# Optimization experiments

Hardware: AMD Instinct MI355X
Metric: run time of the kernel (lower is better)

Reference implementation:

```python
import jax, jax.numpy as jnp
import numpy as np

N_HEAD = 12
N_EMBD = 768

def setup_inputs() -> dict:
    key = jax.random.key(0)
    ks = jax.random.split(key, 5)
    B, T, C = 4, 2048, N_EMBD
    x = jax.random.normal(ks[0], (B, T, C), dtype=jnp.float32)
    # c_attn: Linear(C, 3C); c_proj: Linear(C, C). Torch Linear stores W as [out,in].
    w_attn = jax.random.normal(ks[1], (3 * C, C), dtype=jnp.float32) * (1.0 / np.sqrt(C))
    b_attn = jnp.zeros((3 * C,), dtype=jnp.float32)
    w_proj = jax.random.normal(ks[2], (C, C), dtype=jnp.float32) * (1.0 / np.sqrt(C))
    b_proj = jnp.zeros((C,), dtype=jnp.float32)
    return {"x": x, "w_attn": w_attn, "b_attn": b_attn, "w_proj": w_proj, "b_proj": b_proj}

def reference(x, w_attn, b_attn, w_proj, b_proj):
    B, T, C = x.shape
    H = N_HEAD
    hs = C // H
    qkv = jnp.einsum('btc,oc->bto', x, w_attn) + b_attn  # [B,T,3C]
    q, k, v = jnp.split(qkv, 3, axis=-1)
    # [B,T,C] -> [B,H,T,hs]
    q = q.reshape(B, T, H, hs).transpose(0, 2, 1, 3)
    k = k.reshape(B, T, H, hs).transpose(0, 2, 1, 3)
    v = v.reshape(B, T, H, hs).transpose(0, 2, 1, 3)
    scale = 1.0 / np.sqrt(hs)
    att = jnp.einsum('bhqd,bhkd->bhqk', q, k) * scale  # [B,H,T,T]
    causal = jnp.tril(jnp.ones((T, T), dtype=bool))
    att = jnp.where(causal[None, None], att, -jnp.inf)
    att = jax.nn.softmax(att, axis=-1)
    y = jnp.einsum('bhqk,bhkd->bhqd', att, v)  # [B,H,T,hs]
    y = y.transpose(0, 2, 1, 3).reshape(B, T, C)
    return jnp.einsum('btc,oc->bto', y, w_proj) + b_proj
```

## Files before the change

### kernel.cpp

```cpp
#include <hip/hip_runtime.h>
#include <hip/hip_bf16.h>


typedef __attribute__((ext_vector_type(8))) short bf16x8;
typedef __attribute__((ext_vector_type(4))) short bf16x4;
typedef __attribute__((ext_vector_type(4))) float f32x4;

#define MFMA16(a, b, c) __builtin_amdgcn_mfma_f32_16x16x32_bf16((a), (b), (c), 0, 0, 0)

__device__ __forceinline__ unsigned short f2bfbits(float f) {
  return __builtin_bit_cast(unsigned short, __float2bfloat16(f));
}
__device__ __forceinline__ float bf2f(short b) {
  return __uint_as_float(((unsigned)(unsigned short)b) << 16);
}
__device__ __forceinline__ float fast_exp2(float x) {
#if __has_builtin(__builtin_amdgcn_exp2f)
  return __builtin_amdgcn_exp2f(x);
#else
  return __expf(x * 0.6931471805599453f);
#endif
}
__device__ __forceinline__ float fmax3(float a, float b, float c) {
  return fmaxf(fmaxf(a, b), c);
}
__device__ __forceinline__ unsigned pk2bf(float lo, float hi) {
  return (__builtin_bit_cast(unsigned, hi) & 0xffff0000u) |
         (__builtin_bit_cast(unsigned, lo) >> 16);
}

__device__ __forceinline__ void gload_lds16(const void* g, void* l) {
  __builtin_amdgcn_global_load_lds((const __attribute__((address_space(1))) void*)g,
                                   (__attribute__((address_space(3))) void*)l, 16, 0, 0);
}

__global__ __launch_bounds__(256) void cvt3(const float* __restrict__ x,
                                            const float* __restrict__ wa,
                                            const float* __restrict__ wp,
                                            unsigned short* __restrict__ xb,
                                            unsigned short* __restrict__ wab,
                                            unsigned short* __restrict__ wpb) {
  int i = blockIdx.x * 256 + threadIdx.x;
  const float* in;
  unsigned short* out;
  int j;
  if (i < 1572864) { in = x; out = xb; j = i; }
  else if (i < 2015232) { in = wa; out = wab; j = i - 1572864; }
  else { in = wp; out = wpb; j = i - 2015232; }
  float4 f = ((const float4*)in)[j];
  bf16x4 o;
  o[0] = (short)f2bfbits(f.x); o[1] = (short)f2bfbits(f.y);
  o[2] = (short)f2bfbits(f.z); o[3] = (short)f2bfbits(f.w);
  ((bf16x4*)out)[j] = o;
}

template <typename OutT>
__global__ __launch_bounds__(256) void gemm_bt(const unsigned short* __restrict__ A,
                                               const unsigned short* __restrict__ Bt,
                                               const float* __restrict__ bias,
                                               OutT* __restrict__ C, int M, int N, int K,
                                               int nx, int cpx) {
  __shared__ unsigned short As[128 * 64];
  __shared__ unsigned short Bs[128 * 64];
  const int tid = threadIdx.x;
  const int w = tid >> 6, l = tid & 63;
  const int g = l >> 4, li = l & 15;
  const int wm = w >> 1, wn = w & 1;

  const int bid = blockIdx.x;
  const int swz = (bid & 7) * cpx + (bid >> 3);
  const int bx = swz % nx, by = swz / nx;
  const int m0 = by * 128, n0 = bx * 128;

  const int scw = (l & 7) ^ ((l >> 3) & 7);
  const int swr = li & 7;

  f32x4 acc[4][4] = {};

  for (int kt = 0; kt < K; kt += 64) {
#pragma unroll
    for (int n = 0; n < 4; ++n) {
      int R = w * 32 + n * 8 + (l >> 3);
      gload_lds16(A + (long)(m0 + R) * K + kt + scw * 8, &As[(w * 32 + n * 8) * 64]);
      gload_lds16(Bt + (long)(n0 + R) * K + kt + scw * 8, &Bs[(w * 32 + n * 8) * 64]);
    }
    __syncthreads();
#pragma unroll
    for (int kk = 0; kk < 2; ++kk) {
      bf16x8 a[4], b[4];
#pragma unroll
      for (int m = 0; m < 4; ++m)
        a[m] = *(const bf16x8*)&As[(wm * 64 + m * 16 + li) * 64 + ((kk * 4 + g) ^ swr) * 8];
#pragma unroll
      for (int n = 0; n < 4; ++n)
        b[n] = *(const bf16x8*)&Bs[(wn * 64 + n * 16 + li) * 64 + ((kk * 4 + g) ^ swr) * 8];
#pragma unroll
      for (int m = 0; m < 4; ++m)
#pragma unroll
        for (int n = 0; n < 4; ++n) acc[m][n] = MFMA16(a[m], b[n], acc[m][n]);
    }
    __syncthreads();
  }

#pragma unroll
  for (int m = 0; m < 4; ++m) {
    int row = m0 + wm * 64 + m * 16 + 4 * g;
#pragma unroll
    for (int n = 0; n < 4; ++n) {
      int col = n0 + wn * 64 + n * 16 + li;
      float bi = bias[col];
#pragma unroll
      for (int r = 0; r < 4; ++r) {
        float v = acc[m][n][r] + bi;
        if constexpr (sizeof(OutT) == 2)
          C[(long)(row + r) * N + col] = (OutT)f2bfbits(v);
        else
          C[(long)(row + r) * N + col] = v;
      }
    }
  }
}

__global__ __launch_bounds__(64) void transpose_v(const unsigned short* __restrict__ qkv,
                                                  unsigned short* __restrict__ vt) {
  const int kt = blockIdx.x & 31, bh = blockIdx.x >> 5;
  const int b = bh / 12, h = bh - b * 12;
  const int l = threadIdx.x;
  const int ct = l & 7, cd = l >> 3;

  bf16x8 tin[8], tout[8];
#pragma unroll
  for (int i = 0; i < 8; ++i)
    tin[i] = *(const bf16x8*)(qkv + (long)(b * 2048 + kt * 64 + ct * 8 + i) * 2304 +
                              1536 + h * 64 + cd * 8);
#pragma unroll
  for (int j = 0; j < 8; ++j) {
#pragma unroll
    for (int i = 0; i < 8; ++i) tout[j][i] = tin[i][j];
    *(bf16x8*)(vt + (long)(bh * 64 + cd * 8 + j) * 2048 + kt * 64 + ct * 8) = tout[j];
  }
}

__device__ __forceinline__ bf16x8 scale_bf8(bf16x8 v, float c) {
  bf16x8 o;
#pragma unroll
  for (int j = 0; j < 8; ++j) o[j] = (short)f2bfbits(bf2f(v[j]) * c);
  return o;
}

__device__ __forceinline__ void softmax_state(f32x4* s, bool diag, int g, int li, int qloc,
                                              unsigned short* PsW, float& m, f32x4* o,
                                              f32x4& o4) {
  if (diag) {
#pragma unroll
    for (int kn = 0; kn < 4; ++kn)
#pragma unroll
      for (int r = 0; r < 4; ++r)
        if (kn * 16 + 4 * g + r > qloc) s[kn][r] = -1e30f;
  }
  float a = fmax3(s[0][0], s[0][1], s[0][2]);
  float b = fmax3(s[0][3], s[1][0], s[1][1]);
  float c = fmax3(s[1][2], s[1][3], s[2][0]);
  float d = fmax3(s[2][1], s[2][2], s[2][3]);
  float e = fmax3(s[3][0], s[3][1], s[3][2]);
  float pm = fmaxf(fmax3(a, b, c), fmax3(d, e, s[3][3]));
  pm = fmaxf(pm, __shfl_xor(pm, 16));
  pm = fmaxf(pm, __shfl_xor(pm, 32));

  if (!__all(pm - m <= 10.0f)) {
    float mn = fmaxf(m, pm);
    float alpha = fast_exp2(m - mn);
    m = mn;
    float alo[4];
#pragma unroll
    for (int r = 0; r < 4; ++r) alo[r] = __shfl(alpha, 20 * g + r);
#pragma unroll
    for (int dn = 0; dn < 4; ++dn)
#pragma unroll
      for (int r = 0; r < 4; ++r) o[dn][r] *= alo[r];
#pragma unroll
    for (int r = 0; r < 4; ++r) o4[r] *= alo[r];
  }

  const int swp = li & 7;
#pragma unroll
  for (int kn = 0; kn < 4; ++kn) {
    float e0 = fast_exp2(s[kn][0] - m);
    float e1 = fast_exp2(s[kn][1] - m);
    float e2 = fast_exp2(s[kn][2] - m);
    float e3 = fast_exp2(s[kn][3] - m);
    uint2 pk = {pk2bf(e0, e1), pk2bf(e2, e3)};
    *(uint2*)&PsW[li * 64 + ((kn * 2 + (g >> 1)) ^ swp) * 8 + (g & 1) * 4] = pk;
  }
}

template <bool DUAL>
__device__ __forceinline__ void attn_tile(const unsigned short* Ks, const unsigned short* Vs,
                                          unsigned short* PsH, unsigned short* PsL,
                                          const bf16x8* bqh, const bf16x8* bql,
                                          bool diagh, bool diagl, int g, int li, int qloc,
                                          float& mh, f32x4* oh, f32x4& oh4,
                                          float& ml, f32x4* ol, f32x4& ol4) {
  f32x4 sh[4], sl[4];
  __builtin_amdgcn_s_setprio(1);
#pragma unroll
  for (int kn = 0; kn < 4; ++kn) {
    int rr = kn * 16 + li, sw = rr & 7;
    f32x4 ah = {}, al = {};
#pragma unroll
    for (int kk = 0; kk < 2; ++kk) {
      bf16x8 ak = *(const bf16x8*)&Ks[rr * 64 + ((kk * 4 + g) ^ sw) * 8];
      ah = MFMA16(ak, bqh[kk], ah);
      if constexpr (DUAL) al = MFMA16(ak, bql[kk], al);
    }
    sh[kn] = ah;
    if constexpr (DUAL) sl[kn] = al;
  }
  __builtin_amdgcn_s_setprio(0);

  softmax_state(sh, diagh, g, li, qloc, PsH, mh, oh, oh4);
  if constexpr (DUAL) softmax_state(sl, diagl, g, li, qloc, PsL, ml, ol, ol4);

  bf16x8 vones;
#pragma unroll
  for (int j = 0; j < 8; ++j) vones[j] = (short)0x3F80;

  const int swp = li & 7;
  __builtin_amdgcn_s_setprio(1);
#pragma unroll
  for (int kk = 0; kk < 2; ++kk) {
    bf16x8 pah = *(const bf16x8*)&PsH[li * 64 + ((kk * 4 + g) ^ swp) * 8];
    bf16x8 pal;
    if constexpr (DUAL) pal = *(const bf16x8*)&PsL[li * 64 + ((kk * 4 + g) ^ swp) * 8];
#pragma unroll
    for (int dn = 0; dn < 4; ++dn) {
      int rv = dn * 16 + li;
      bf16x8 vb = *(const bf16x8*)&Vs[rv * 64 + ((kk * 4 + g) ^ (rv & 7)) * 8];
      oh[dn] = MFMA16(pah, vb, oh[dn]);
      if constexpr (DUAL) ol[dn] = MFMA16(pal, vb, ol[dn]);
    }
    oh4 = MFMA16(pah, vones, oh4);
    if constexpr (DUAL) ol4 = MFMA16(pal, vones, ol4);
  }
  __builtin_amdgcn_s_setprio(0);
}

__global__ __launch_bounds__(256, 3) void attn_fwd(const unsigned short* __restrict__ qkv,
                                                   const unsigned short* __restrict__ vt,
                                                   unsigned short* __restrict__ y) {
  const int orig = (blockIdx.x & 7) * 96 + (blockIdx.x >> 3);
  const int bh = orig >> 4, p = orig & 15;
  const int b = bh / 12, h = bh - b * 12;
  const int qlo = p, qhi = 31 - p;
  const int tid = threadIdx.x;
  const int w = tid >> 6, l = tid & 63;
  const int g = l >> 4, li = l & 15;
  const int qloc = w * 16 + li;

  __shared__ unsigned short Ks[2][64 * 64];
  __shared__ unsigned short Vs[2][64 * 64];
  __shared__ unsigned short Ps[8][16 * 64];
  unsigned short* PsH = &Ps[w][0];
  unsigned short* PsL = &Ps[4 + w][0];

  const unsigned short* base = qkv + (long)b * 2048 * 2304;

  const float QS = 0.18033688011112042f;
  bf16x8 bqlo[2], bqhi[2];
  {
    const unsigned short* qr = base + (long)(qlo * 64 + qloc) * 2304 + h * 64;
    bqlo[0] = scale_bf8(*(const bf16x8*)(qr + 8 * g), QS);
    bqlo[1] = scale_bf8(*(const bf16x8*)(qr + 32 + 8 * g), QS);
    qr = base + (long)(qhi * 64 + qloc) * 2304 + h * 64;
    bqhi[0] = scale_bf8(*(const bf16x8*)(qr + 8 * g), QS);
    bqhi[1] = scale_bf8(*(const bf16x8*)(qr + 32 + 8 * g), QS);
  }

  float m_lo = -1e30f, m_hi = -1e30f;
  f32x4 o_lo[4] = {}, o_hi[4] = {};
  f32x4 o4_lo = {}, o4_hi = {};

  const int sR = w * 8 + (l >> 3);
  const int sc = l & 7;

  int buf = 0;
  {
#pragma unroll
    for (int n = 0; n < 2; ++n) {
      int R = n * 32 + sR;
      int c = sc ^ (R & 7);
      gload_lds16(base + (long)R * 2304 + 768 + h * 64 + c * 8, &Ks[0][(n * 32 + w * 8) * 64]);
      gload_lds16(vt + (long)(bh * 64 + R) * 2048 + c * 8, &Vs[0][(n * 32 + w * 8) * 64]);
    }
  }
  __syncthreads();

  for (int kt = 0; kt <= qhi; ++kt) {
    if (kt < qhi) {
#pragma unroll
      for (int n = 0; n < 2; ++n) {
        int R = n * 32 + sR;
        int c = sc ^ (R & 7);
        gload_lds16(base + (long)((kt + 1) * 64 + R) * 2304 + 768 + h * 64 + c * 8,
                    &Ks[buf ^ 1][(n * 32 + w * 8) * 64]);
        gload_lds16(vt + (long)(bh * 64 + R) * 2048 + (kt + 1) * 64 + c * 8,
                    &Vs[buf ^ 1][(n * 32 + w * 8) * 64]);
      }
    }
    if (kt <= qlo)
      attn_tile<true>(Ks[buf], Vs[buf], PsH, PsL, bqhi, bqlo, kt == qhi, kt == qlo,
                      g, li, qloc, m_hi, o_hi, o4_hi, m_lo, o_lo, o4_lo);
    else
      attn_tile<false>(Ks[buf], Vs[buf], PsH, PsL, bqhi, bqlo, kt == qhi, false,
                       g, li, qloc, m_hi, o_hi, o4_hi, m_lo, o_lo, o4_lo);
    __syncthreads();
    buf ^= 1;
  }

#pragma unroll
  for (int t = 0; t < 2; ++t) {
    const f32x4* o = t ? o_hi : o_lo;
    const f32x4& o4 = t ? o4_hi : o4_lo;
    int qt = t ? qhi : qlo;
#pragma unroll
    for (int r = 0; r < 4; ++r) {
      float inv = 1.0f / o4[r];
      long row = (long)b * 2048 + qt * 64 + w * 16 + 4 * g + r;
#pragma unroll
      for (int dn = 0; dn < 4; ++dn)
        y[row * 768 + h * 64 + dn * 16 + li] = (unsigned short)f2bfbits(o[dn][r] * inv);
    }
  }
}

extern "C" void kernel_launch(void* const* d_in, const int* in_sizes, int n_in,
                              void* d_out, int out_size, void* d_ws, size_t ws_size,
                              hipStream_t stream) {
  const float* x      = (const float*)d_in[0];
  const float* w_attn = (const float*)d_in[1];
  const float* b_attn = (const float*)d_in[2];
  const float* w_proj = (const float*)d_in[3];
  const float* b_proj = (const float*)d_in[4];
  float* out = (float*)d_out;

  unsigned short* xb   = (unsigned short*)d_ws;
  unsigned short* wab  = xb + 6291456;
  unsigned short* wpb  = wab + 1769472;
  unsigned short* qkvb = wpb + 589824;
  unsigned short* yb   = qkvb + (long)8192 * 2304;
  unsigned short* vtb  = yb + 6291456;

  cvt3<<<8448, 256, 0, stream>>>(x, w_attn, w_proj, xb, wab, wpb);

  gemm_bt<unsigned short><<<1152, 256, 0, stream>>>(xb, wab, b_attn, qkvb, 8192, 2304, 768, 18, 144);
  transpose_v<<<1536, 64, 0, stream>>>(qkvb, vtb);
  attn_fwd<<<768, 256, 0, stream>>>(qkvb, vtb, yb);
  gemm_bt<float><<<384, 256, 0, stream>>>(yb, wpb, b_proj, out, 8192, 768, 768, 6, 48);
}
```

Before: 135.4 us.

## Fuse V transpose into QKV GEMM epilogue and remap attention block schedule

The QKV GEMM epilogue now writes V-column tiles straight into the transposed V layout, so the separate transpose kernel and its extra read/write of V are gone. The attention kernel's block-to-(head, query-pair) mapping is also changed: each XCD now gets six contiguous heads, and the query-pair index is rotated to spread the causal workload. The fused epilogue writes 4-element bf16 chunks along the time axis, which may coalesce less well than the old writes.

```diff
diff --git a/kernel.cpp b/kernel.cpp
--- a/kernel.cpp
+++ b/kernel.cpp
@@ -54,12 +54,13 @@
   ((bf16x4*)out)[j] = o;
 }
 
-template <typename OutT>
+template <typename OutT, bool VFUSE>
 __global__ __launch_bounds__(256) void gemm_bt(const unsigned short* __restrict__ A,
                                                const unsigned short* __restrict__ Bt,
                                                const float* __restrict__ bias,
-                                               OutT* __restrict__ C, int M, int N, int K,
-                                               int nx, int cpx) {
+                                               OutT* __restrict__ C,
+                                               unsigned short* __restrict__ vt,
+                                               int M, int N, int K, int nx, int cpx) {
   __shared__ unsigned short As[128 * 64];
   __shared__ unsigned short Bs[128 * 64];
   const int tid = threadIdx.x;
@@ -100,6 +101,29 @@
         for (int n = 0; n < 4; ++n) acc[m][n] = MFMA16(a[m], b[n], acc[m][n]);
     }
     __syncthreads();
+  }
+
+  if constexpr (VFUSE) {
+    if (n0 >= 1536) {
+      const int b = m0 >> 11;
+      const int t0b = (m0 & 2047) + wm * 64;
+#pragma unroll
+      for (int n = 0; n < 4; ++n) {
+        int col = n0 + wn * 64 + n * 16 + li;
+        int h = (col - 1536) >> 6, d = (col - 1536) & 63;
+        float bi = bias[col];
+        long vrow = ((long)(b * 12 + h) * 64 + d) * 2048;
+#pragma unroll
+        for (int m = 0; m < 4; ++m) {
+          int t0 = t0b + m * 16 + 4 * g;
+          bf16x4 pk;
+#pragma unroll
+          for (int r = 0; r < 4; ++r) pk[r] = (short)f2bfbits(acc[m][n][r] + bi);
+          *(bf16x4*)&vt[vrow + t0] = pk;
+        }
+      }
+      return;
+    }
   }
 
 #pragma unroll
@@ -118,26 +142,6 @@
           C[(long)(row + r) * N + col] = v;
       }
     }
-  }
-}
-
-__global__ __launch_bounds__(64) void transpose_v(const unsigned short* __restrict__ qkv,
-                                                  unsigned short* __restrict__ vt) {
-  const int kt = blockIdx.x & 31, bh = blockIdx.x >> 5;
-  const int b = bh / 12, h = bh - b * 12;
-  const int l = threadIdx.x;
-  const int ct = l & 7, cd = l >> 3;
-
-  bf16x8 tin[8], tout[8];
-#pragma unroll
-  for (int i = 0; i < 8; ++i)
-    tin[i] = *(const bf16x8*)(qkv + (long)(b * 2048 + kt * 64 + ct * 8 + i) * 2304 +
-                              1536 + h * 64 + cd * 8);
-#pragma unroll
-  for (int j = 0; j < 8; ++j) {
-#pragma unroll
-    for (int i = 0; i < 8; ++i) tout[j][i] = tin[i][j];
-    *(bf16x8*)(vt + (long)(bh * 64 + cd * 8 + j) * 2048 + kt * 64 + ct * 8) = tout[j];
   }
 }
 
@@ -248,8 +252,10 @@
 __global__ __launch_bounds__(256, 3) void attn_fwd(const unsigned short* __restrict__ qkv,
                                                    const unsigned short* __restrict__ vt,
                                                    unsigned short* __restrict__ y) {
-  const int orig = (blockIdx.x & 7) * 96 + (blockIdx.x >> 3);
-  const int bh = orig >> 4, p = orig & 15;
+  const int xcd = blockIdx.x & 7;
+  const int slot = blockIdx.x >> 3;
+  const int bh = xcd * 6 + (slot >> 4);
+  const int p = ((slot & 15) + 11 * (slot >> 5)) & 15;
   const int b = bh / 12, h = bh - b * 12;
   const int qlo = p, qhi = 31 - p;
   const int tid = threadIdx.x;
@@ -352,8 +358,9 @@
 
   cvt3<<<8448, 256, 0, stream>>>(x, w_attn, w_proj, xb, wab, wpb);
 
-  gemm_bt<unsigned short><<<1152, 256, 0, stream>>>(xb, wab, b_attn, qkvb, 8192, 2304, 768, 18, 144);
-  transpose_v<<<1536, 64, 0, stream>>>(qkvb, vtb);
+  gemm_bt<unsigned short, true><<<1152, 256, 0, stream>>>(xb, wab, b_attn, qkvb, vtb,
+                                                          8192, 2304, 768, 18, 144);
   attn_fwd<<<768, 256, 0, stream>>>(qkvb, vtb, yb);
-  gemm_bt<float><<<384, 256, 0, stream>>>(yb, wpb, b_proj, out, 8192, 768, 768, 6, 48);
-}
+  gemm_bt<float, false><<<384, 256, 0, stream>>>(yb, wpb, b_proj, out, nullptr,
+                                                 8192, 768, 768, 6, 48);
+}
```

Measured after the change: 138.5 us. +2.3%, slower.

## Process lo/hi query tiles sequentially with shared P buffer and remap block schedule

Applied to the files above, without the earlier changes.

Replaces the interleaved dual-tile attention step with two sequential calls of a single-tile routine that share one P scratch buffer per wave. This halves the P shared memory and lowers register pressure from holding two score sets at once. The cost is losing interleaved MFMA issue between the two query tiles and re-reading K/V fragments from LDS. The block-to-(bh, pair) mapping is also changed so each XCD handles contiguous heads with rotated pair indices, aiming at better L2 locality and load balance.

```diff
diff --git a/kernel.cpp b/kernel.cpp
--- a/kernel.cpp
+++ b/kernel.cpp
@@ -194,53 +194,41 @@
   }
 }
 
-template <bool DUAL>
-__device__ __forceinline__ void attn_tile(const unsigned short* Ks, const unsigned short* Vs,
-                                          unsigned short* PsH, unsigned short* PsL,
-                                          const bf16x8* bqh, const bf16x8* bql,
-                                          bool diagh, bool diagl, int g, int li, int qloc,
-                                          float& mh, f32x4* oh, f32x4& oh4,
-                                          float& ml, f32x4* ol, f32x4& ol4) {
-  f32x4 sh[4], sl[4];
+__device__ __forceinline__ void attn_state(const unsigned short* Ks, const unsigned short* Vs,
+                                           unsigned short* PsW, const bf16x8* bq, bool diag,
+                                           int g, int li, int qloc,
+                                           float& m, f32x4* o, f32x4& o4) {
+  f32x4 s[4];
   __builtin_amdgcn_s_setprio(1);
 #pragma unroll
   for (int kn = 0; kn < 4; ++kn) {
     int rr = kn * 16 + li, sw = rr & 7;
-    f32x4 ah = {}, al = {};
+    f32x4 acc = {};
 #pragma unroll
     for (int kk = 0; kk < 2; ++kk) {
       bf16x8 ak = *(const bf16x8*)&Ks[rr * 64 + ((kk * 4 + g) ^ sw) * 8];
-      ah = MFMA16(ak, bqh[kk], ah);
-      if constexpr (DUAL) al = MFMA16(ak, bql[kk], al);
-    }
-    sh[kn] = ah;
-    if constexpr (DUAL) sl[kn] = al;
+      acc = MFMA16(ak, bq[kk], acc);
+    }
+    s[kn] = acc;
   }
   __builtin_amdgcn_s_setprio(0);
 
-  softmax_state(sh, diagh, g, li, qloc, PsH, mh, oh, oh4);
-  if constexpr (DUAL) softmax_state(sl, diagl, g, li, qloc, PsL, ml, ol, ol4);
+  softmax_state(s, diag, g, li, qloc, PsW, m, o, o4);
 
   bf16x8 vones;
 #pragma unroll
   for (int j = 0; j < 8; ++j) vones[j] = (short)0x3F80;
-
   const int swp = li & 7;
   __builtin_amdgcn_s_setprio(1);
 #pragma unroll
   for (int kk = 0; kk < 2; ++kk) {
-    bf16x8 pah = *(const bf16x8*)&PsH[li * 64 + ((kk * 4 + g) ^ swp) * 8];
-    bf16x8 pal;
-    if constexpr (DUAL) pal = *(const bf16x8*)&PsL[li * 64 + ((kk * 4 + g) ^ swp) * 8];
+    bf16x8 pa = *(const bf16x8*)&PsW[li * 64 + ((kk * 4 + g) ^ swp) * 8];
 #pragma unroll
     for (int dn = 0; dn < 4; ++dn) {
-      int rv = dn * 16 + li;
-      bf16x8 vb = *(const bf16x8*)&Vs[rv * 64 + ((kk * 4 + g) ^ (rv & 7)) * 8];
-      oh[dn] = MFMA16(pah, vb, oh[dn]);
-      if constexpr (DUAL) ol[dn] = MFMA16(pal, vb, ol[dn]);
-    }
-    oh4 = MFMA16(pah, vones, oh4);
-    if constexpr (DUAL) ol4 = MFMA16(pal, vones, ol4);
+      bf16x8 vb = *(const bf16x8*)&Vs[(dn * 16 + li) * 64 + ((kk * 4 + g) ^ swp) * 8];
+      o[dn] = MFMA16(pa, vb, o[dn]);
+    }
+    o4 = MFMA16(pa, vones, o4);
   }
   __builtin_amdgcn_s_setprio(0);
 }
@@ -248,8 +236,10 @@
 __global__ __launch_bounds__(256, 3) void attn_fwd(const unsigned short* __restrict__ qkv,
                                                    const unsigned short* __restrict__ vt,
                                                    unsigned short* __restrict__ y) {
-  const int orig = (blockIdx.x & 7) * 96 + (blockIdx.x >> 3);
-  const int bh = orig >> 4, p = orig & 15;
+  const int xcd = blockIdx.x & 7;
+  const int slot = blockIdx.x >> 3;
+  const int bh = xcd * 6 + (slot >> 4);
+  const int p = ((slot & 15) + 11 * (slot >> 5)) & 15;
   const int b = bh / 12, h = bh - b * 12;
   const int qlo = p, qhi = 31 - p;
   const int tid = threadIdx.x;
@@ -259,9 +249,8 @@
 
   __shared__ unsigned short Ks[2][64 * 64];
   __shared__ unsigned short Vs[2][64 * 64];
-  __shared__ unsigned short Ps[8][16 * 64];
-  unsigned short* PsH = &Ps[w][0];
-  unsigned short* PsL = &Ps[4 + w][0];
+  __shared__ unsigned short Ps[4][16 * 64];
+  unsigned short* PsW = &Ps[w][0];
 
   const unsigned short* base = qkv + (long)b * 2048 * 2304;
 
@@ -307,12 +296,9 @@
                     &Vs[buf ^ 1][(n * 32 + w * 8) * 64]);
       }
     }
+    attn_state(Ks[buf], Vs[buf], PsW, bqhi, kt == qhi, g, li, qloc, m_hi, o_hi, o4_hi);
     if (kt <= qlo)
-      attn_tile<true>(Ks[buf], Vs[buf], PsH, PsL, bqhi, bqlo, kt == qhi, kt == qlo,
-                      g, li, qloc, m_hi, o_hi, o4_hi, m_lo, o_lo, o4_lo);
-    else
-      attn_tile<false>(Ks[buf], Vs[buf], PsH, PsL, bqhi, bqlo, kt == qhi, false,
-                       g, li, qloc, m_hi, o_hi, o4_hi, m_lo, o_lo, o4_lo);
+      attn_state(Ks[buf], Vs[buf], PsW, bqlo, kt == qlo, g, li, qloc, m_lo, o_lo, o4_lo);
     __syncthreads();
     buf ^= 1;
   }
```

New measurement: 130.2 us. -3.8%, faster.
